# Kernel optimization log

Measured on AMD Instinct MI355X. Metric: run time of the kernel, lower is better.

## Reference

```python
import jax, jax.numpy as jnp
import numpy as np

DIM_IN = 256
DIM_H = 64


def setup_inputs() -> dict:
    key = jax.random.key(0)
    ks = jax.random.split(key, 7)
    s = 1.0 / np.sqrt(DIM_IN + DIM_H)  # torch Linear default init scale
    inp = {
        "inputs": jax.random.normal(ks[0], (256, 512, DIM_IN), dtype=jnp.float32),
        # weights stored as (in_features, out_features) for x @ W
        "W_input": jax.random.uniform(ks[1], (DIM_IN + DIM_H, DIM_H), minval=-s, maxval=s, dtype=jnp.float32),
        "b_input": jax.random.uniform(ks[2], (DIM_H,), minval=-s, maxval=s, dtype=jnp.float32),
        "W_update": jax.random.uniform(ks[3], (DIM_IN + DIM_H, DIM_H), minval=-s, maxval=s, dtype=jnp.float32),
        "b_update": jax.random.uniform(ks[4], (DIM_H,), minval=-s, maxval=s, dtype=jnp.float32),
        "W_reset": jax.random.uniform(ks[5], (DIM_IN + DIM_H, DIM_H), minval=-s, maxval=s, dtype=jnp.float32),
        "b_reset": jax.random.uniform(ks[6], (DIM_H,), minval=-s, maxval=s, dtype=jnp.float32),
    }
    return inp


def reference(inputs, W_input, b_input, W_update, b_update, W_reset, b_reset):
    batch = inputs.shape[0]

    # Split each (dim_in+H, H) weight into its input-part and hidden-part so we
    # avoid per-step concatenation: cat([x, h]) @ W == x @ Wx + h @ Wh.
    Wi_x, Wi_h = W_input[:DIM_IN], W_input[DIM_IN:]
    Wu_x, Wu_h = W_update[:DIM_IN], W_update[DIM_IN:]
    Wr_x, Wr_h = W_reset[:DIM_IN], W_reset[DIM_IN:]

    # Precompute all input-side projections in one big GEMM: [B, L, H]
    xu = jnp.einsum('bld,dh->blh', inputs, Wu_x) + b_update
    xr = jnp.einsum('bld,dh->blh', inputs, Wr_x) + b_reset
    xi = jnp.einsum('bld,dh->blh', inputs, Wi_x) + b_input

    def step(h_prev, xs):
        xu_t, xr_t, xi_t = xs  # each [B, H]
        z = jax.nn.sigmoid(xu_t + h_prev @ Wu_h)
        r = jax.nn.sigmoid(xr_t + h_prev @ Wr_h)
        h_next = (1.0 - z) * h_prev + z * jnp.tanh(xi_t + (h_prev * r) @ Wi_h)
        return h_next, h_next

    h0 = jnp.zeros((batch, DIM_H), dtype=inputs.dtype)
    xs = (jnp.swapaxes(xu, 0, 1), jnp.swapaxes(xr, 0, 1), jnp.swapaxes(xi, 0, 1))  # [L, B, H]
    _, outs = jax.lax.scan(step, h0, xs)
    return jnp.swapaxes(outs, 0, 1)  # [B, L, H]
```

## Files before the change

kernel.cpp:

```cpp
#include <hip/hip_runtime.h>

#define DIM_IN 256
#define DIM_H  64
#define SEQ_LEN 512
#define TPB 4

typedef _Float16 h2_t  __attribute__((ext_vector_type(2)));
typedef _Float16 h8_t  __attribute__((ext_vector_type(8)));
typedef float    f32x4 __attribute__((ext_vector_type(4)));
union H8 { h8_t v; h2_t p[4]; };

typedef const __attribute__((address_space(1))) unsigned* gcu32_p;
typedef const __attribute__((address_space(1))) _Float16* gch16_p;
typedef const __attribute__((address_space(1))) float*    gcf32_p;
typedef       __attribute__((address_space(1))) float*    gf32_p;

__device__ inline float dot2(h2_t a, h2_t b, float c) {
#if __has_builtin(__builtin_amdgcn_fdot2)
    return __builtin_amdgcn_fdot2(a, b, c, false);
#else
    return c + (float)a[0] * (float)b[0] + (float)a[1] * (float)b[1];
#endif
}
__device__ inline float exp2_(float x) {
#if __has_builtin(__builtin_amdgcn_exp2f)
    return __builtin_amdgcn_exp2f(x);
#else
    return exp2f(x);
#endif
}
__device__ inline float rcp_(float x) {
#if __has_builtin(__builtin_amdgcn_rcpf)
    return __builtin_amdgcn_rcpf(x);
#else
    return __fdividef(1.f, x);
#endif
}

#define LDS_FENCE() __asm__ volatile("s_waitcnt lgkmcnt(0)" ::: "memory")

template <int XI16>
__global__ __launch_bounds__(256, 2)
void gru_prepass_mfma(const float* __restrict__ X,
                      const float* __restrict__ W_input,  const float* __restrict__ b_input,
                      const float* __restrict__ W_update, const float* __restrict__ b_update,
                      const float* __restrict__ W_reset,  const float* __restrict__ b_reset,
                      unsigned* __restrict__ xur_out,
                      _Float16* __restrict__ xi16_out, float* __restrict__ xi32_out)
{
    const int tid  = threadIdx.x;
    const int lane = tid & 63;
    const int wv   = tid >> 6;
    const int q    = lane >> 4;
    const int m16  = lane & 15;

    constexpr int LDK = DIM_IN + 8;
    __shared__ _Float16 xs[64 * LDK];

    const int c = wv * 16 + m16;
    h8_t bu[8], brf[8], bif[8];
#pragma unroll
    for (int kt = 0; kt < 8; ++kt) {
        h8_t u, r, i;
#pragma unroll
        for (int jj = 0; jj < 8; ++jj) {
            const int k = kt * 32 + q * 8 + jj;
            u[jj] = (_Float16)W_update[k * DIM_H + c];
            r[jj] = (_Float16)W_reset [k * DIM_H + c];
            i[jj] = (_Float16)W_input [k * DIM_H + c];
        }
        bu[kt] = u; brf[kt] = r; bif[kt] = i;
    }
    const float bzc = b_update[c], brc = b_reset[c], bic = b_input[c];

    const int tile0 = blockIdx.x * TPB;
    float4 pf[16];
    {
        const float4* xb = (const float4*)(X + (size_t)tile0 * 64 * DIM_IN);
#pragma unroll
        for (int i = 0; i < 16; ++i) pf[i] = xb[tid + 256 * i];
    }

#pragma unroll 1
    for (int tI = 0; tI < TPB; ++tI) {
#pragma unroll
        for (int i = 0; i < 16; ++i) {
            const int f   = tid + 256 * i;
            const int row = f >> 6;
            const int kq  = f & 63;
            const float4 v = pf[i];
            h2_t a, b2;
            a[0]  = (_Float16)v.x; a[1]  = (_Float16)v.y;
            b2[0] = (_Float16)v.z; b2[1] = (_Float16)v.w;
            _Float16* dst = &xs[row * LDK + kq * 4];
            *(h2_t*)dst = a; *(h2_t*)(dst + 2) = b2;
        }
        __syncthreads();
        if (tI + 1 < TPB) {
            const float4* xb = (const float4*)(X + (size_t)(tile0 + tI + 1) * 64 * DIM_IN);
#pragma unroll
            for (int i = 0; i < 16; ++i) pf[i] = xb[tid + 256 * i];
        }
        const size_t orow0 = (size_t)(tile0 + tI) * 64;
#pragma unroll
        for (int rt = 0; rt < 4; ++rt) {
            const int r0 = rt * 16;
            f32x4 au = {0.f,0.f,0.f,0.f}, ar = {0.f,0.f,0.f,0.f}, aa = {0.f,0.f,0.f,0.f};
#pragma unroll
            for (int kt = 0; kt < 8; ++kt) {
                const h8_t a = *(const h8_t*)&xs[(r0 + m16) * LDK + kt * 32 + q * 8];
                au = __builtin_amdgcn_mfma_f32_16x16x32_f16(a, bu[kt],  au, 0, 0, 0);
                ar = __builtin_amdgcn_mfma_f32_16x16x32_f16(a, brf[kt], ar, 0, 0, 0);
                aa = __builtin_amdgcn_mfma_f32_16x16x32_f16(a, bif[kt], aa, 0, 0, 0);
            }
#pragma unroll
            for (int i = 0; i < 4; ++i) {
                const size_t grow = orow0 + r0 + q * 4 + i;
                h2_t pk;
                pk[0] = (_Float16)(-1.44269504f * (au[i] + bzc));
                pk[1] = (_Float16)(-1.44269504f * (ar[i] + brc));
                xur_out[grow * DIM_H + c] = __builtin_bit_cast(unsigned, pk);
                const float xiv = 2.88539008f * (aa[i] + bic);
                if (XI16) xi16_out[grow * DIM_H + c] = (_Float16)xiv;
                else      xi32_out[grow * DIM_H + c] = xiv;
            }
        }
        __syncthreads();
    }
}


#define DOTR(HX, Q)                                                 \
    ar0 = dot2(HX.p[0], wr[4*(Q)+0], ar0);                          \
    ar1 = dot2(HX.p[1], wr[4*(Q)+1], ar1);                          \
    ar2 = dot2(HX.p[2], wr[4*(Q)+2], ar2);                          \
    ar3 = dot2(HX.p[3], wr[4*(Q)+3], ar3);

#define DOTZ(HX, Q)                                                 \
    az0 = dot2(HX.p[0], wu[4*(Q)+0], az0);                          \
    az1 = dot2(HX.p[1], wu[4*(Q)+1], az1);                          \
    az2 = dot2(HX.p[2], wu[4*(Q)+2], az2);                          \
    az3 = dot2(HX.p[3], wu[4*(Q)+3], az3);

#define DOTI(SX, Q)                                                 \
    ax0 = dot2(SX.p[0], wi[4*(Q)+0], ax0);                          \
    ax1 = dot2(SX.p[1], wi[4*(Q)+1], ax1);                          \
    ax2 = dot2(SX.p[2], wi[4*(Q)+2], ax2);                          \
    ax3 = dot2(SX.p[3], wi[4*(Q)+3], ax3);

template <int XI16>
__global__
__attribute__((amdgpu_flat_work_group_size(64, 64)))
__attribute__((amdgpu_waves_per_eu(1, 1)))
void gru_rec(const unsigned* __restrict__ xur, const _Float16* __restrict__ xi16,
             const float* __restrict__ xif,
             const float* __restrict__ W_input, const float* __restrict__ W_update,
             const float* __restrict__ W_reset,
             float* __restrict__ out)
{
    const int b = blockIdx.x;
    const int j = threadIdx.x;

    __shared__ __align__(16) _Float16 hh[DIM_H];
    __shared__ __align__(16) _Float16 ss[DIM_H];

    h2_t wu[32], wr[32], wi[32];
#pragma unroll
    for (int m = 0; m < 32; ++m) {
        const int k = DIM_IN + 2 * m;
        h2_t a, cc, d;
        a[0]  = (_Float16)W_update[(k    ) * DIM_H + j];
        a[1]  = (_Float16)W_update[(k + 1) * DIM_H + j];
        cc[0] = (_Float16)W_reset [(k    ) * DIM_H + j];
        cc[1] = (_Float16)W_reset [(k + 1) * DIM_H + j];
        d[0]  = (_Float16)W_input [(k    ) * DIM_H + j];
        d[1]  = (_Float16)W_input [(k + 1) * DIM_H + j];
        wu[m] = a; wr[m] = cc; wi[m] = d;
    }

    hh[j] = (_Float16)0.f;
    float hprev = 0.f;

    const size_t base = (size_t)b * SEQ_LEN * DIM_H + j;
    gcu32_p xg  = (gcu32_p)(xur + base);
    gch16_p ig  = (gch16_p)(xi16 + base);
    gcf32_p igf = (gcf32_p)(xif + base);
    gf32_p  og  = (gf32_p)(out + base);

    unsigned ru[8];
    float    rxi[8];
#pragma unroll
    for (int d = 0; d < 8; ++d) {
        ru[d]  = xg[(size_t)d * DIM_H];
        rxi[d] = XI16 ? (float)ig[(size_t)d * DIM_H] : igf[(size_t)d * DIM_H];
    }
    LDS_FENCE();

#pragma unroll 1
    for (int tb = 0; tb < SEQ_LEN / 8; ++tb) {
#pragma unroll
        for (int u = 0; u < 8; ++u) {
            const int t = tb * 8 + u;
            const h2_t pr = __builtin_bit_cast(h2_t, ru[u]);
            const float xu = (float)pr[0];
            const float xr = (float)pr[1];
            const float xi = rxi[u];
            const int tp = (t + 8 < SEQ_LEN) ? t + 8 : SEQ_LEN - 1;
            ru[u]  = xg[(size_t)tp * DIM_H];
            rxi[u] = XI16 ? (float)ig[(size_t)tp * DIM_H] : igf[(size_t)tp * DIM_H];

            const H8* hp = (const H8*)hh;
            H8 hx0 = hp[0], hx1 = hp[1], hx2 = hp[2], hx3 = hp[3],
               hx4 = hp[4], hx5 = hp[5], hx6 = hp[6], hx7 = hp[7];

            float ar0 = 0.f, ar1 = 0.f, ar2 = 0.f, ar3 = 0.f;
            DOTR(hx0,0) DOTR(hx1,1) DOTR(hx2,2) DOTR(hx3,3)
            DOTR(hx4,4) DOTR(hx5,5) DOTR(hx6,6) DOTR(hx7,7)
            const float rg = rcp_(1.f + exp2_(
                fmaf((ar0 + ar1) + (ar2 + ar3), -1.44269504f, xr)));
            ss[j] = (_Float16)(hprev * rg);
            LDS_FENCE();

            const H8* sp = (const H8*)ss;
            H8 sx0 = sp[0], sx1 = sp[1], sx2 = sp[2], sx3 = sp[3],
               sx4 = sp[4], sx5 = sp[5], sx6 = sp[6], sx7 = sp[7];

            float az0 = 0.f, az1 = 0.f, az2 = 0.f, az3 = 0.f;
            DOTZ(hx0,0) DOTZ(hx1,1) DOTZ(hx2,2) DOTZ(hx3,3)
            DOTZ(hx4,4) DOTZ(hx5,5) DOTZ(hx6,6) DOTZ(hx7,7)
            const float zg = rcp_(1.f + exp2_(
                fmaf((az0 + az1) + (az2 + az3), -1.44269504f, xu)));

            float ax0 = 0.f, ax1 = 0.f, ax2 = 0.f, ax3 = 0.f;
            DOTI(sx0,0) DOTI(sx1,1) DOTI(sx2,2) DOTI(sx3,3)
            DOTI(sx4,4) DOTI(sx5,5) DOTI(sx6,6) DOTI(sx7,7)
            const float th = fmaf(-2.f, rcp_(1.f + exp2_(
                fmaf((ax0 + ax1) + (ax2 + ax3), 2.88539008f, xi))), 1.f);

            const float hn = fmaf(zg, th - hprev, hprev);
            hh[j] = (_Float16)hn;
            LDS_FENCE();
            og[(size_t)t * DIM_H] = hn;
            hprev = hn;
        }
    }
}

extern "C" void kernel_launch(void* const* d_in, const int* in_sizes, int n_in,
                              void* d_out, int out_size, void* d_ws, size_t ws_size,
                              hipStream_t stream) {
    const float* inputs   = (const float*)d_in[0];
    const float* W_input  = (const float*)d_in[1];
    const float* b_input  = (const float*)d_in[2];
    const float* W_update = (const float*)d_in[3];
    const float* b_update = (const float*)d_in[4];
    const float* W_reset  = (const float*)d_in[5];
    const float* b_reset  = (const float*)d_in[6];
    float* out = (float*)d_out;

    const int    batch = in_sizes[0] / (SEQ_LEN * DIM_IN);
    const size_t rows  = (size_t)batch * SEQ_LEN;
    const int    nblk  = (int)(rows / 64 / TPB);

    unsigned* xur_w = (unsigned*)d_ws;
    _Float16* xi_w  = (_Float16*)(xur_w + rows * DIM_H);
    const bool xi16 = ws_size >= rows * DIM_H * 6ull;

    if (xi16) {
        gru_prepass_mfma<1><<<nblk, 256, 0, stream>>>(
            inputs, W_input, b_input, W_update, b_update, W_reset, b_reset,
            xur_w, xi_w, out);
        gru_rec<1><<<batch, 64, 0, stream>>>(xur_w, xi_w, out,
                                             W_input, W_update, W_reset, out);
    } else {
        gru_prepass_mfma<0><<<nblk, 256, 0, stream>>>(
            inputs, W_input, b_input, W_update, b_update, W_reset, b_reset,
            xur_w, xi_w, out);
        gru_rec<0><<<batch, 64, 0, stream>>>(xur_w, xi_w, out,
                                             W_input, W_update, W_reset, out);
    }
}
```

Before: 422.5 us.

## Broadcast hidden state via DPP and readlane instead of LDS round-trips

Replaces the shared-memory exchange of the hidden state and reset-scaled state with a DPP swap that packs neighbouring fp16 values into pairs, followed by 32 readlane broadcasts into scalar registers. This removes LDS stores, loads and waitcnt fences from the serial per-timestep dependency chain. In exchange, each step issues 64 readlane instructions, which serialize on instruction issue and carry VALU-to-SGPR hazard stalls. The dot-product accumulation is also restructured to use more independent accumulators.

```diff
diff --git a/kernel.cpp b/kernel.cpp
--- a/kernel.cpp
+++ b/kernel.cpp
@@ -8,7 +8,6 @@
 typedef _Float16 h2_t  __attribute__((ext_vector_type(2)));
 typedef _Float16 h8_t  __attribute__((ext_vector_type(8)));
 typedef float    f32x4 __attribute__((ext_vector_type(4)));
-union H8 { h8_t v; h2_t p[4]; };
 
 typedef const __attribute__((address_space(1))) unsigned* gcu32_p;
 typedef const __attribute__((address_space(1))) _Float16* gch16_p;
@@ -36,8 +35,6 @@
     return __fdividef(1.f, x);
 #endif
 }
-
-#define LDS_FENCE() __asm__ volatile("s_waitcnt lgkmcnt(0)" ::: "memory")
 
 template <int XI16>
 __global__ __launch_bounds__(256, 2)
@@ -130,39 +127,28 @@
 }
 
 
-#define DOTR(HX, Q)                                                 \
-    ar0 = dot2(HX.p[0], wr[4*(Q)+0], ar0);                          \
-    ar1 = dot2(HX.p[1], wr[4*(Q)+1], ar1);                          \
-    ar2 = dot2(HX.p[2], wr[4*(Q)+2], ar2);                          \
-    ar3 = dot2(HX.p[3], wr[4*(Q)+3], ar3);
-
-#define DOTZ(HX, Q)                                                 \
-    az0 = dot2(HX.p[0], wu[4*(Q)+0], az0);                          \
-    az1 = dot2(HX.p[1], wu[4*(Q)+1], az1);                          \
-    az2 = dot2(HX.p[2], wu[4*(Q)+2], az2);                          \
-    az3 = dot2(HX.p[3], wu[4*(Q)+3], az3);
-
-#define DOTI(SX, Q)                                                 \
-    ax0 = dot2(SX.p[0], wi[4*(Q)+0], ax0);                          \
-    ax1 = dot2(SX.p[1], wi[4*(Q)+1], ax1);                          \
-    ax2 = dot2(SX.p[2], wi[4*(Q)+2], ax2);                          \
-    ax3 = dot2(SX.p[3], wi[4*(Q)+3], ax3);
+__device__ inline void bcast_pairs(float v, unsigned (&dst)[32]) {
+    const unsigned lo = (unsigned)__builtin_bit_cast(unsigned short, (_Float16)v);
+    const unsigned nb = (unsigned)__builtin_amdgcn_update_dpp(
+        0, (int)lo, 0xB1 , 0xF, 0xF, true);
+    const unsigned pair = lo | (nb << 16);
+#pragma unroll
+    for (int m = 0; m < 32; ++m)
+        dst[m] = (unsigned)__builtin_amdgcn_readlane((int)pair, 2 * m);
+}
 
 template <int XI16>
 __global__
 __attribute__((amdgpu_flat_work_group_size(64, 64)))
 __attribute__((amdgpu_waves_per_eu(1, 1)))
 void gru_rec(const unsigned* __restrict__ xur, const _Float16* __restrict__ xi16,
-             const float* __restrict__ xif,
+             const float* xif,
              const float* __restrict__ W_input, const float* __restrict__ W_update,
              const float* __restrict__ W_reset,
              float* __restrict__ out)
 {
     const int b = blockIdx.x;
     const int j = threadIdx.x;
-
-    __shared__ __align__(16) _Float16 hh[DIM_H];
-    __shared__ __align__(16) _Float16 ss[DIM_H];
 
     h2_t wu[32], wr[32], wi[32];
 #pragma unroll
@@ -178,14 +164,16 @@
         wu[m] = a; wr[m] = cc; wi[m] = d;
     }
 
-    hh[j] = (_Float16)0.f;
     float hprev = 0.f;
+    unsigned hp[32];
+#pragma unroll
+    for (int m = 0; m < 32; ++m) hp[m] = 0u;
 
     const size_t base = (size_t)b * SEQ_LEN * DIM_H + j;
-    gcu32_p xg  = (gcu32_p)(xur + base);
+    gcu32_p xg  = (gcu32_p)(xur  + base);
     gch16_p ig  = (gch16_p)(xi16 + base);
-    gcf32_p igf = (gcf32_p)(xif + base);
-    gf32_p  og  = (gf32_p)(out + base);
+    gcf32_p igf = (gcf32_p)(xif  + base);
+    gf32_p  og  = (gf32_p)(out  + base);
 
     unsigned ru[8];
     float    rxi[8];
@@ -194,7 +182,6 @@
         ru[d]  = xg[(size_t)d * DIM_H];
         rxi[d] = XI16 ? (float)ig[(size_t)d * DIM_H] : igf[(size_t)d * DIM_H];
     }
-    LDS_FENCE();
 
 #pragma unroll 1
     for (int tb = 0; tb < SEQ_LEN / 8; ++tb) {
@@ -209,38 +196,39 @@
             ru[u]  = xg[(size_t)tp * DIM_H];
             rxi[u] = XI16 ? (float)ig[(size_t)tp * DIM_H] : igf[(size_t)tp * DIM_H];
 
-            const H8* hp = (const H8*)hh;
-            H8 hx0 = hp[0], hx1 = hp[1], hx2 = hp[2], hx3 = hp[3],
-               hx4 = hp[4], hx5 = hp[5], hx6 = hp[6], hx7 = hp[7];
-
-            float ar0 = 0.f, ar1 = 0.f, ar2 = 0.f, ar3 = 0.f;
-            DOTR(hx0,0) DOTR(hx1,1) DOTR(hx2,2) DOTR(hx3,3)
-            DOTR(hx4,4) DOTR(hx5,5) DOTR(hx6,6) DOTR(hx7,7)
-            const float rg = rcp_(1.f + exp2_(
-                fmaf((ar0 + ar1) + (ar2 + ar3), -1.44269504f, xr)));
-            ss[j] = (_Float16)(hprev * rg);
-            LDS_FENCE();
-
-            const H8* sp = (const H8*)ss;
-            H8 sx0 = sp[0], sx1 = sp[1], sx2 = sp[2], sx3 = sp[3],
-               sx4 = sp[4], sx5 = sp[5], sx6 = sp[6], sx7 = sp[7];
-
-            float az0 = 0.f, az1 = 0.f, az2 = 0.f, az3 = 0.f;
-            DOTZ(hx0,0) DOTZ(hx1,1) DOTZ(hx2,2) DOTZ(hx3,3)
-            DOTZ(hx4,4) DOTZ(hx5,5) DOTZ(hx6,6) DOTZ(hx7,7)
-            const float zg = rcp_(1.f + exp2_(
-                fmaf((az0 + az1) + (az2 + az3), -1.44269504f, xu)));
-
-            float ax0 = 0.f, ax1 = 0.f, ax2 = 0.f, ax3 = 0.f;
-            DOTI(sx0,0) DOTI(sx1,1) DOTI(sx2,2) DOTI(sx3,3)
-            DOTI(sx4,4) DOTI(sx5,5) DOTI(sx6,6) DOTI(sx7,7)
-            const float th = fmaf(-2.f, rcp_(1.f + exp2_(
-                fmaf((ax0 + ax1) + (ax2 + ax3), 2.88539008f, xi))), 1.f);
+            float arA[8] = {0.f,0.f,0.f,0.f,0.f,0.f,0.f,0.f};
+            float azA[4] = {0.f,0.f,0.f,0.f};
+#pragma unroll
+            for (int m = 0; m < 32; ++m) {
+                const h2_t a = __builtin_bit_cast(h2_t, hp[m]);
+                arA[m & 7] = dot2(a, wr[m], arA[m & 7]);
+                azA[m & 3] = dot2(a, wu[m], azA[m & 3]);
+            }
+            const float drs = ((arA[0]+arA[4]) + (arA[1]+arA[5]))
+                            + ((arA[2]+arA[6]) + (arA[3]+arA[7]));
+            const float rg  = rcp_(1.f + exp2_(fmaf(drs, -1.44269504f, xr)));
+
+            unsigned sp[32];
+            bcast_pairs(hprev * rg, sp);
+
+            const float dzs = (azA[0] + azA[1]) + (azA[2] + azA[3]);
+            const float zg  = rcp_(1.f + exp2_(fmaf(dzs, -1.44269504f, xu)));
+
+            float axA[8] = {0.f,0.f,0.f,0.f,0.f,0.f,0.f,0.f};
+#pragma unroll
+            for (int m = 0; m < 32; ++m) {
+                const h2_t a = __builtin_bit_cast(h2_t, sp[m]);
+                axA[m & 7] = dot2(a, wi[m], axA[m & 7]);
+            }
+            const float dxs = ((axA[0]+axA[4]) + (axA[1]+axA[5]))
+                            + ((axA[2]+axA[6]) + (axA[3]+axA[7]));
+            const float th  = fmaf(-2.f, rcp_(1.f + exp2_(
+                                  fmaf(dxs, 2.88539008f, xi))), 1.f);
 
             const float hn = fmaf(zg, th - hprev, hprev);
-            hh[j] = (_Float16)hn;
-            LDS_FENCE();
             og[(size_t)t * DIM_H] = hn;
+
+            bcast_pairs(hn, hp);
             hprev = hn;
         }
     }
```

Result: slower. 442.6 us (+4.8%).
